# Optimization experiments

Measured on AMD Instinct MI355X. Metric: run time of the kernel, lower is better.

## Reference

```python
import jax, jax.numpy as jnp
import numpy as np
from fractions import Fraction
from math import factorial

# ---------- e3nn-convention real Wigner 3j (computed once in numpy) ----------

def _su2_cg(j1, m1, j2, m2, j3, m3):
    if m3 != m1 + m2:
        return 0.0
    vmin = int(max(-j1 + j2 + m3, -j1 + m1, 0))
    vmax = int(min(j2 + j3 + m1, j3 - j1 + j2, j3 + m3))
    f = lambda n: factorial(round(n))
    C = ((2.0 * j3 + 1.0) * Fraction(
        f(j3 + j1 - j2) * f(j3 - j1 + j2) * f(j1 + j2 - j3) * f(j3 + m3) * f(j3 - m3),
        f(j1 + j2 + j3 + 1) * f(j1 - m1) * f(j1 + m1) * f(j2 - m2) * f(j2 + m2))) ** 0.5
    S = 0
    for v in range(vmin, vmax + 1):
        S += (-1) ** int(v + j2 + m2) * Fraction(
            f(j2 + j3 + m1 - v) * f(j1 - m1 + v),
            f(v) * f(j3 - j1 + j2 - v) * f(j3 + m3 - v) * f(v + j1 - j2 - m3))
    return float(C * S)

def _q_real2complex(l):
    q = np.zeros((2 * l + 1, 2 * l + 1), dtype=complex)
    for m in range(-l, 0):
        q[l + m, l + abs(m)] = 1 / 2 ** 0.5
        q[l + m, l - abs(m)] = -1j / 2 ** 0.5
    q[l, l] = 1.0
    for m in range(1, l + 1):
        q[l + m, l + abs(m)] = (-1) ** m / 2 ** 0.5
        q[l + m, l - abs(m)] = 1j * (-1) ** m / 2 ** 0.5
    return (-1j) ** l * q

def _w3j(l1, l2, l3):
    C = np.zeros((2 * l1 + 1, 2 * l2 + 1, 2 * l3 + 1), dtype=complex)
    for m1 in range(-l1, l1 + 1):
        for m2 in range(-l2, l2 + 1):
            for m3 in range(-l3, l3 + 1):
                C[l1 + m1, l2 + m2, l3 + m3] = _su2_cg(l1, m1, l2, m2, l3, m3)
    C = np.einsum('ij,kl,mn,ikn->jlm', _q_real2complex(l1), _q_real2complex(l2),
                  np.conj(_q_real2complex(l3).T), C)
    assert np.abs(C.imag).max() < 1e-7
    C = C.real
    return C / np.linalg.norm(C)

# uuw instructions from get_feasible_tp(hidden, hidden, 0e+1e+2e): (l1, l2, l_out)
INS = [(0, 0, 0), (0, 2, 2), (1, 1, 0), (1, 1, 1), (1, 1, 2), (2, 0, 2), (2, 2, 0), (2, 2, 1), (2, 2, 2)]
W3J = {ls: jnp.asarray(_w3j(*ls), dtype=jnp.float32) for ls in set(INS)}
# change of basis of ReducedTensorProducts('ij', i='1o'): sph(0e+1e+2e) -> cart 3x3
Q_COB = jnp.asarray(np.concatenate([(2 * l + 1) ** 0.5 * _w3j(1, 1, l).transpose(2, 0, 1)
                                    for l in (0, 1, 2)], axis=0), dtype=jnp.float32)  # (9,3,3)
IN_IRR = ((128, 0), (64, 1), (32, 2))  # edge_irreps, dim 480
HID = 16                               # hidden multiplicity per l
CART = jnp.array([2, 0, 1])            # e3nn (y,z,x) -> (x,y,z)

def _split(x):
    parts, o = [], 0
    for mul, l in IN_IRR:
        d = mul * (2 * l + 1)
        parts.append(x[:, o:o + d].reshape(-1, mul, 2 * l + 1))
        o += d
    return parts

def _lin(parts, Ws):  # e3nn o3.Linear: per-l channel mix, 1/sqrt(fan_in)
    return [jnp.einsum('nui,uv->nvi', p, W) * (1.0 / np.sqrt(p.shape[1])) for p, W in zip(parts, Ws)]

def _forward(batch, x_scalar, x_spherical, WU0, WU1, WU2, WV0, WV1, WV2,
             Wg1, bg1, Wg2, bg2, Wp0, Wp1, Wp2, num_graphs):
    xs = _split(x_spherical)
    hU = _lin(xs, (WU0, WU1, WU2))  # [(N,16,1),(N,16,3),(N,16,5)]
    hV = _lin(xs, (WV0, WV1, WV2))
    w = jax.nn.silu(x_scalar @ Wg1 + bg1) @ Wg2 + bg2  # (N, 144) per-path tp weights
    outs = {0: [], 1: [], 2: []}
    for k, (l1, l2, l3) in enumerate(INS):
        wk = w[:, k * HID:(k + 1) * HID]
        coeff = float(np.sqrt((2 * l3 + 1) / HID))  # component/element norm
        outs[l3].append(coeff * jnp.einsum('nu,ijm,nui,nuj->nm', wk, W3J[(l1, l2, l3)], hU[l1], hV[l2]))
    Wp = {0: Wp0, 1: Wp1, 2: Wp2}
    sph = [jnp.einsum('num,u->nm', jnp.stack(outs[l], 1), Wp[l][:, 0]) * (1.0 / np.sqrt(len(outs[l])))
           for l in (0, 1, 2)]  # lin_out_post -> 1x0e+1x1e+1x2e
    atom_out = jnp.concatenate(sph, axis=-1)  # (N, 9)
    res_sph = jax.ops.segment_sum(atom_out, batch, num_segments=num_graphs)  # (G, 9)
    res_cart = jnp.einsum('gk,kij->gij', res_sph, Q_COB)  # (G, 3, 3)
    return res_cart[:, CART][:, :, CART]

def setup_inputs():
    key = jax.random.key(0)
    k = jax.random.split(key, 16)
    N, G = 150000, 2000
    f32 = jnp.float32
    rn = lambda kk, shp, s=1.0: jax.random.normal(kk, shp, f32) * s
    return {
        'batch': jnp.sort(jax.random.randint(k[0], (N,), 0, G)),
        'x_scalar': rn(k[1], (N, 128)),
        'x_spherical': rn(k[2], (N, 480)),
        'WU0': rn(k[3], (128, 16)), 'WU1': rn(k[4], (64, 16)), 'WU2': rn(k[5], (32, 16)),
        'WV0': rn(k[6], (128, 16)), 'WV1': rn(k[7], (64, 16)), 'WV2': rn(k[8], (32, 16)),
        'Wg1': rn(k[9], (128, 64), 128 ** -0.5), 'bg1': jnp.zeros((64,), f32),
        'Wg2': rn(k[10], (64, 144), 64 ** -0.5), 'bg2': jnp.zeros((144,), f32),
        'Wp0': rn(k[11], (3, 1)), 'Wp1': rn(k[12], (2, 1)), 'Wp2': rn(k[13], (4, 1)),
        'num_graphs': G,
    }

def reference(batch, x_scalar, x_spherical, WU0, WU1, WU2, WV0, WV1, WV2,
              Wg1, bg1, Wg2, bg2, Wp0, Wp1, Wp2, num_graphs):
    return _forward(batch, x_scalar, x_spherical, WU0, WU1, WU2, WV0, WV1, WV2,
                    Wg1, bg1, Wg2, bg2, Wp0, Wp1, Wp2, num_graphs)
```

## Files before the change

kernel.cpp:

```cpp
#include <hip/hip_runtime.h>
#include <hip/hip_bf16.h>
#include <math.h>

typedef unsigned short u16;
typedef unsigned int   u32;
typedef __attribute__((ext_vector_type(8))) short short8v;
typedef __attribute__((ext_vector_type(4))) float f32x4;

#define TILE 16

#define WS_FLAG  368
#define WS_MOK   369
#define WS_WG1   384
#define WS_WG2   8576
#define WS_WU0   17792
#define WS_WU1   19840
#define WS_WU2   20864
#define WS_WV0   21376
#define WS_WV1   23424
#define WS_WV2   24448
#define WS_BG1   24960
#define WS_BG2   25024
#define WS_C9    25168
#define WS_RES   25216

#define WSH_BG1T 88064
#define WSH_BG2T 96256
#define WSH_B0T  105472
#define WSH_B1T  109568
#define WSH_B2T  128000
#define WS_NEED_BYTES 307200

__device__ __forceinline__ float b2f(u16 u){
  return __uint_as_float(((u32)u) << 16);
}
__device__ __forceinline__ u16 f2b(float f){
  u32 x = __float_as_uint(f);
  return (u16)((x + 0x7fffu + ((x >> 16) & 1u)) >> 16);
}
__device__ __forceinline__ float ldconv(const void* p, int i, int isbf){
  return isbf ? b2f(((const u16*)p)[i]) : ((const float*)p)[i];
}

__global__ void detect_kernel(const u32* __restrict__ words, int* __restrict__ flag){
  int t = threadIdx.x;
  int cnt = 0;
  for (int i = 0; i < 16; i++){
    u32 w = words[t*16 + i];
    u32 e = (w >> 7) & 0xFF;
    cnt += (e >= 117 && e <= 137) ? 1 : 0;
  }
  #pragma unroll
  for (int m = 1; m < 64; m <<= 1) cnt += __shfl_xor(cnt, m, 64);
  if (t == 0) *flag = (cnt > 512) ? 1 : 0;
}

__device__ double factd(int n){ double r=1.0; for(int i=2;i<=n;++i) r*=(double)i; return r; }

__device__ double su2_cg(int j1,int m1,int j2,int m2,int j3,int m3){
  if (m1+m2 != m3) return 0.0;
  int vmin = max(max(-j1+j2+m3, -j1+m1), 0);
  int vmax = min(min(j2+j3+m1, j3-j1+j2), j3+m3);
  double C = sqrt((2.0*j3+1.0)
      * factd(j3+j1-j2)*factd(j3-j1+j2)*factd(j1+j2-j3)*factd(j3+m3)*factd(j3-m3)
      / (factd(j1+j2+j3+1)*factd(j1-m1)*factd(j1+m1)*factd(j2-m2)*factd(j2+m2)));
  double S = 0.0;
  for (int v=vmin; v<=vmax; ++v){
    double t = factd(j2+j3+m1-v)*factd(j1-m1+v)
             / (factd(v)*factd(j3-j1+j2-v)*factd(j3+m3-v)*factd(v+j1-j2-m3));
    S += ((v+j2+m2)&1) ? -t : t;
  }
  return C*S;
}

__device__ void qmat_lds(int l, double* qre, double* qim){
  int d = 2*l+1;
  for (int i=0;i<d*d;i++){ qre[i]=0.0; qim[i]=0.0; }
  double s = 1.0/sqrt(2.0);
  for (int m=-l; m<0; ++m){
    qre[(l+m)*d + (l-m)] = s;
    qim[(l+m)*d + (l+m)] = -s;
  }
  qre[l*d + l] = 1.0;
  for (int m=1; m<=l; ++m){
    double sgn = (m&1) ? -1.0 : 1.0;
    qre[(l+m)*d + (l+m)] = sgn*s;
    qim[(l+m)*d + (l-m)] = sgn*s;
  }
  double fr, fi;
  switch (l & 3){ case 0: fr=1; fi=0; break; case 1: fr=0; fi=-1; break;
                  case 2: fr=-1; fi=0; break; default: fr=0; fi=1; }
  for (int i=0;i<d*d;i++){
    double a=qre[i], b=qim[i];
    qre[i]=a*fr-b*fi; qim[i]=a*fi+b*fr;
  }
}

__global__ void setup_kernel(float* __restrict__ ws){
  __shared__ double q1r[25], q1i[25], q2r[25], q2i[25], q3r[25], q3i[25];
  __shared__ double red[128];
  const int L1[9]={0,0,1,1,1,2,2,2,2};
  const int L2[9]={0,2,1,1,1,0,2,2,2};
  const int L3[9]={0,2,0,1,2,2,0,1,2};
  const int OFF[9]={0,1,26,35,62,107,132,157,232};
  const int b = blockIdx.x;
  const int l1=L1[b], l2=L2[b], l3=L3[b];
  const int d1=2*l1+1, d2=2*l2+1, d3=2*l3+1;
  const int tot = d1*d2*d3;
  const int t = threadIdx.x;

  if (t==0) qmat_lds(l1, q1r, q1i);
  if (t==1) qmat_lds(l2, q2r, q2i);
  if (t==2) qmat_lds(l3, q3r, q3i);
  __syncthreads();

  double ar = 0.0;
  if (t < tot){
    const int j = t/(d2*d3), rem = t - j*(d2*d3), l = rem/d3, m = rem - l*d3;
    for (int i=0;i<d1;i++){
      double a1r=q1r[i*d1+j], a1i=q1i[i*d1+j];
      for (int k=0;k<d2;k++){
        double a2r=q2r[k*d2+l], a2i=q2i[k*d2+l];
        double t12r = a1r*a2r - a1i*a2i;
        double t12i = a1r*a2i + a1i*a2r;
        for (int n=0;n<d3;n++){
          double c = su2_cg(l1, i-l1, l2, k-l2, l3, n-l3);
          if (c==0.0) continue;
          double a3r = q3r[n*d3+m], a3i = -q3i[n*d3+m];
          ar += c*(t12r*a3r - t12i*a3i);
        }
      }
    }
  }
  red[t] = ar*ar;
  __syncthreads();
  for (int s=64; s>0; s>>=1){
    if (t < s) red[t] += red[t+s];
    __syncthreads();
  }
  double nrm = sqrt(red[0]);
  if (t < tot) ws[OFF[b] + t] = (float)(ar/nrm);
}

__global__ void convert_weights(
    const void* Wg1, const void* Wg2,
    const void* WU0, const void* WU1, const void* WU2,
    const void* WV0, const void* WV1, const void* WV2,
    const void* bg1, const void* bg2,
    const void* Wp0, const void* Wp1, const void* Wp2,
    float* __restrict__ ws)
{
  const int isbf = ((const int*)ws)[WS_FLAG];
  const int b = blockIdx.x, t = threadIdx.x;
  u16* wh = (u16*)ws;
  if (b < 10){
    const void* src[10] = {Wg1,Wg2,WU0,WU1,WU2,WV0,WV1,WV2,bg1,bg2};
    const int   sz[10]  = {8192,9216,2048,1024,512,2048,1024,512,64,144};
    const int   off[10] = {WS_WG1,WS_WG2,WS_WU0,WS_WU1,WS_WU2,WS_WV0,WS_WV1,WS_WV2,WS_BG1,WS_BG2};
    const void* s = src[b]; float* d = ws + off[b]; int n = sz[b];
    for (int i = t; i < n; i += 256) d[i] = ldconv(s, i, isbf);
  } else if (b == 10){
    if (t == 0){
      float* C9 = ws + WS_C9;
      const int l3k[9]  = {0,2,0,1,2,2,0,1,2};
      const int idxk[9] = {0,0,1,0,1,2,2,1,3};
      for (int k=0;k<9;k++){
        int l3 = l3k[k];
        const void* wp = (l3==0) ? Wp0 : (l3==1) ? Wp1 : Wp2;
        float wpv = ldconv(wp, idxk[k], isbf);
        float len = (l3==0) ? 3.f : (l3==1) ? 2.f : 4.f;
        C9[k] = sqrtf((2.f*l3 + 1.f)/16.f) * wpv * rsqrtf(len);
      }
    }
  } else if (b == 11){
    for (int i=t;i<8192;i+=256){
      int n = i >> 7, k = i & 127;
      wh[WSH_BG1T + i] = f2b(ldconv(Wg1, k*64 + n, isbf));
    }
  } else if (b == 12){
    for (int i=t;i<9216;i+=256){
      int n = i >> 6, k = i & 63;
      wh[WSH_BG2T + i] = f2b(ldconv(Wg2, k*144 + n, isbf));
    }
  } else if (b == 13){
    for (int i=t;i<4096;i+=256){
      int n = i >> 7, k = i & 127;
      float v = (n < 16) ? ldconv(WU0, k*16 + n, isbf)
                         : ldconv(WV0, k*16 + (n-16), isbf);
      wh[WSH_B0T + i] = f2b(v);
    }
  } else if (b == 14){
    for (int i=t;i<18432;i+=256){
      int n = i / 192, k = i - n*192;
      int uv = n / 48, rem = n - uv*48, ii = rem >> 4, vv = rem & 15;
      float val = 0.f;
      if (k % 3 == ii){
        int u = k / 3;
        val = ldconv(uv ? WV1 : WU1, u*16 + vv, isbf);
      }
      wh[WSH_B1T + i] = f2b(val);
    }
  } else if (b == 15){
    for (int i=t;i<25600;i+=256){
      int n = i / 160, k = i - n*160;
      int uv = n / 80, rem = n - uv*80, ii = rem >> 4, vv = rem & 15;
      float val = 0.f;
      if (k % 5 == ii){
        int u = k / 5;
        val = ldconv(uv ? WV2 : WU2, u*16 + vv, isbf);
      }
      wh[WSH_B2T + i] = f2b(val);
    }
  }
}

__global__ void probe_kernel(float* __restrict__ ws){
  __shared__ u16 A[512];
  __shared__ u16 B[512];
  int t = threadIdx.x;
  for (int i=t;i<512;i+=64){
    int m = i >> 5, k = i & 31;
    A[i] = f2b((float)(((3*m + k) % 7) - 3));
    int kk = i >> 4, n = i & 15;
    B[i] = f2b((float)(((2*kk + 5*n) % 9) - 4));
  }
  __syncthreads();
  int v = t & 15, g4 = t >> 4;
  short8v a, b;
  #pragma unroll
  for (int j=0;j<8;j++){
    a[j] = (short)A[v*32 + 8*g4 + j];
    b[j] = (short)B[(8*g4 + j)*16 + v];
  }
  f32x4 c = {0.f,0.f,0.f,0.f};
  c = __builtin_amdgcn_mfma_f32_16x16x32_bf16(a, b, c, 0, 0, 0);
  int ok = 1;
  #pragma unroll
  for (int r=0;r<4;r++){
    int row = 4*g4 + r;
    float ref = 0.f;
    for (int k=0;k<32;k++) ref += b2f(A[row*32+k]) * b2f(B[k*16+v]);
    if (fabsf(c[r] - ref) > 0.25f) ok = 0;
  }
  #pragma unroll
  for (int m=1;m<64;m<<=1) ok &= __shfl_xor(ok, m, 64);
  if (t == 0) ((int*)ws)[WS_MOK] = ok;
}

__global__ __launch_bounds__(256,3) void mfma_kernel(
    const int* __restrict__ batch,
    const void* __restrict__ xscv,
    const void* __restrict__ xspv,
    const float* __restrict__ ws,
    float* __restrict__ res,
    int N)
{
  const int isbf = ((const int*)ws)[WS_FLAG];
  const int mok  = ((const int*)ws)[WS_MOK];
  if (!(isbf && mok)) return;

  __shared__ __align__(16) u16 H1hi[4][16][72];
  __shared__ __align__(16) u16 H1lo[4][16][72];

  const int tid = threadIdx.x;
  const int wave = tid >> 6, lane = tid & 63;
  const int v = lane & 15, g4 = lane >> 4;
  const int tile = blockIdx.x*4 + wave;
  const int n0 = tile * TILE;
  if (n0 >= N) return;

  const u16* xsc = (const u16*)xscv;
  const u16* xsp = (const u16*)xspv;
  const u16* wb  = (const u16*)ws;

  int rowA = n0 + v; if (rowA >= N) rowA = N - 1;

  f32x4 accg[4];
  #pragma unroll
  for (int nt=0;nt<4;nt++) accg[nt] = (f32x4){0.f,0.f,0.f,0.f};
  {
    const u16* aP = xsc + (size_t)rowA*128 + 8*g4;
    const u16* bP = wb + WSH_BG1T + v*128 + 8*g4;
    #pragma unroll
    for (int kt=0;kt<4;kt++){
      short8v a = *(const short8v*)(aP + kt*32);
      #pragma unroll
      for (int nt=0;nt<4;nt++){
        short8v b = *(const short8v*)(bP + nt*2048 + kt*32);
        accg[nt] = __builtin_amdgcn_mfma_f32_16x16x32_bf16(a, b, accg[nt], 0, 0, 0);
      }
    }
  }
  #pragma unroll
  for (int nt=0;nt<4;nt++){
    float bb = ws[WS_BG1 + nt*16 + v];
    #pragma unroll
    for (int r=0;r<4;r++){
      float hs = accg[nt][r] + bb;
      float h  = hs / (1.f + __expf(-hs));
      u16 hi = f2b(h);
      float lo = h - b2f(hi);
      int atom = 4*g4 + r;
      H1hi[wave][atom][nt*16 + v] = hi;
      H1lo[wave][atom][nt*16 + v] = f2b(lo);
    }
  }

  f32x4 accw[9];
  #pragma unroll
  for (int nt=0;nt<9;nt++) accw[nt] = (f32x4){0.f,0.f,0.f,0.f};
  {
    const u16* hH = &H1hi[wave][v][8*g4];
    const u16* hL = &H1lo[wave][v][8*g4];
    const u16* bP = wb + WSH_BG2T + v*64 + 8*g4;
    #pragma unroll
    for (int kt=0;kt<2;kt++){
      short8v ah = *(const short8v*)(hH + kt*32);
      short8v al = *(const short8v*)(hL + kt*32);
      #pragma unroll
      for (int nt=0;nt<9;nt++){
        short8v b = *(const short8v*)(bP + nt*1024 + kt*32);
        accw[nt] = __builtin_amdgcn_mfma_f32_16x16x32_bf16(ah, b, accw[nt], 0, 0, 0);
        accw[nt] = __builtin_amdgcn_mfma_f32_16x16x32_bf16(al, b, accw[nt], 0, 0, 0);
      }
    }
  }
  float wkv[9][4];
  #pragma unroll
  for (int nt=0;nt<9;nt++){
    float bb = ws[WS_BG2 + nt*16 + v];
    float c9 = ws[WS_C9 + nt];
    #pragma unroll
    for (int r=0;r<4;r++) wkv[nt][r] = (accw[nt][r] + bb) * c9;
  }

  const u16* spA = xsp + (size_t)rowA*480 + 8*g4;

  f32x4 acc0[2];
  #pragma unroll
  for (int nt=0;nt<2;nt++) acc0[nt] = (f32x4){0.f,0.f,0.f,0.f};
  {
    const u16* bP = wb + WSH_B0T + v*128 + 8*g4;
    #pragma unroll
    for (int kt=0;kt<4;kt++){
      short8v a = *(const short8v*)(spA + kt*32);
      #pragma unroll
      for (int nt=0;nt<2;nt++){
        short8v b = *(const short8v*)(bP + nt*2048 + kt*32);
        acc0[nt] = __builtin_amdgcn_mfma_f32_16x16x32_bf16(a, b, acc0[nt], 0, 0, 0);
      }
    }
  }
  f32x4 accA[6];
  #pragma unroll
  for (int nt=0;nt<6;nt++) accA[nt] = (f32x4){0.f,0.f,0.f,0.f};
  {
    const u16* bP = wb + WSH_B1T + v*192 + 8*g4;
    #pragma unroll
    for (int kt=0;kt<6;kt++){
      short8v a = *(const short8v*)(spA + 128 + kt*32);
      #pragma unroll
      for (int nt=0;nt<6;nt++){
        short8v b = *(const short8v*)(bP + nt*3072 + kt*32);
        accA[nt] = __builtin_amdgcn_mfma_f32_16x16x32_bf16(a, b, accA[nt], 0, 0, 0);
      }
    }
  }
  f32x4 accB[10];
  #pragma unroll
  for (int nt=0;nt<10;nt++) accB[nt] = (f32x4){0.f,0.f,0.f,0.f};
  {
    const u16* bP = wb + WSH_B2T + v*160 + 8*g4;
    #pragma unroll
    for (int kt=0;kt<5;kt++){
      short8v a = *(const short8v*)(spA + 320 + kt*32);
      #pragma unroll
      for (int nt=0;nt<10;nt++){
        short8v b = *(const short8v*)(bP + nt*2560 + kt*32);
        accB[nt] = __builtin_amdgcn_mfma_f32_16x16x32_bf16(a, b, accB[nt], 0, 0, 0);
      }
    }
  }

  int bidr[4];
  #pragma unroll
  for (int r=0;r<4;r++){
    int n = n0 + 4*g4 + r;
    bidr[r] = (n < N) ? batch[n] : -1;
  }

  const float r128 = 0.088388347648318447f;
  const float r64  = 0.125f;
  const float r32  = 0.17677669529663689f;
  const float* J = ws;
  float pend[9];
  int pg = -1;

  #pragma unroll
  for (int r=0;r<4;r++){
    float hu0 = acc0[0][r]*r128, hv0 = acc0[1][r]*r128;
    float hu1[3], hv1[3], hu2[5], hv2[5];
    #pragma unroll
    for (int i=0;i<3;i++){ hu1[i] = accA[i][r]*r64; hv1[i] = accA[3+i][r]*r64; }
    #pragma unroll
    for (int i=0;i<5;i++){ hu2[i] = accB[i][r]*r32; hv2[i] = accB[5+i][r]*r32; }

    float t9[9] = {0,0,0,0,0,0,0,0,0};
    t9[0] += wkv[0][r]*J[0]*hu0*hv0;
    {
      float cw = wkv[1][r]*hu0;
      #pragma unroll
      for (int m=0;m<5;m++){
        float s=0.f;
        #pragma unroll
        for (int j=0;j<5;j++) s += J[1 + j*5 + m]*hv2[j];
        t9[4+m] += cw*s;
      }
    }
    {
      float s=0.f;
      #pragma unroll
      for (int i=0;i<3;i++)
        #pragma unroll
        for (int j=0;j<3;j++) s += J[26 + i*3 + j]*hu1[i]*hv1[j];
      t9[0] += wkv[2][r]*s;
    }
    {
      float sm[3]={0,0,0};
      #pragma unroll
      for (int i=0;i<3;i++)
        #pragma unroll
        for (int j=0;j<3;j++){
          float p = hu1[i]*hv1[j];
          #pragma unroll
          for (int m=0;m<3;m++) sm[m] += J[35 + (i*3+j)*3 + m]*p;
        }
      #pragma unroll
      for (int m=0;m<3;m++) t9[1+m] += wkv[3][r]*sm[m];
    }
    {
      float sm[5]={0,0,0,0,0};
      #pragma unroll
      for (int i=0;i<3;i++)
        #pragma unroll
        for (int j=0;j<3;j++){
          float p = hu1[i]*hv1[j];
          #pragma unroll
          for (int m=0;m<5;m++) sm[m] += J[62 + (i*3+j)*5 + m]*p;
        }
      #pragma unroll
      for (int m=0;m<5;m++) t9[4+m] += wkv[4][r]*sm[m];
    }
    {
      float cw = wkv[5][r]*hv0;
      #pragma unroll
      for (int m=0;m<5;m++){
        float s=0.f;
        #pragma unroll
        for (int i=0;i<5;i++) s += J[107 + i*5 + m]*hu2[i];
        t9[4+m] += cw*s;
      }
    }
    {
      float s=0.f;
      #pragma unroll
      for (int i=0;i<5;i++)
        #pragma unroll
        for (int j=0;j<5;j++) s += J[132 + i*5 + j]*hu2[i]*hv2[j];
      t9[0] += wkv[6][r]*s;
    }
    {
      float sm[3]={0,0,0};
      #pragma unroll
      for (int i=0;i<5;i++)
        #pragma unroll
        for (int j=0;j<5;j++){
          float p = hu2[i]*hv2[j];
          #pragma unroll
          for (int m=0;m<3;m++) sm[m] += J[157 + (i*5+j)*3 + m]*p;
        }
      #pragma unroll
      for (int m=0;m<3;m++) t9[1+m] += wkv[7][r]*sm[m];
    }
    {
      float sm[5]={0,0,0,0,0};
      #pragma unroll
      for (int i=0;i<5;i++)
        #pragma unroll
        for (int j=0;j<5;j++){
          float p = hu2[i]*hv2[j];
          #pragma unroll
          for (int m=0;m<5;m++) sm[m] += J[232 + (i*5+j)*5 + m]*p;
        }
      #pragma unroll
      for (int m=0;m<5;m++) t9[4+m] += wkv[8][r]*sm[m];
    }

    #pragma unroll
    for (int mask=1; mask<16; mask<<=1){
      #pragma unroll
      for (int s=0;s<9;s++) t9[s] += __shfl_xor(t9[s], mask, 64);
    }
    if (v == 0){
      int n = n0 + 4*g4 + r;
      if (n < N){
        int g = bidr[r];
        if (g == pg){
          #pragma unroll
          for (int s=0;s<9;s++) pend[s] += t9[s];
        } else {
          if (pg >= 0){
            float* rp = res + (size_t)pg*9;
            #pragma unroll
            for (int s=0;s<9;s++) atomicAdd(&rp[s], pend[s]);
          }
          pg = g;
          #pragma unroll
          for (int s=0;s<9;s++) pend[s] = t9[s];
        }
      }
    }
  }
  if (v == 0 && pg >= 0){
    float* rp = res + (size_t)pg*9;
    #pragma unroll
    for (int s=0;s<9;s++) atomicAdd(&rp[s], pend[s]);
  }
}

__device__ __forceinline__ void load8_bf16(const u16* p, float* dst){
  uint4 vv = *reinterpret_cast<const uint4*>(p);
  u32 w[4] = {vv.x, vv.y, vv.z, vv.w};
  #pragma unroll
  for (int q=0;q<4;q++){
    dst[2*q]   = __uint_as_float((w[q] & 0xffffu) << 16);
    dst[2*q+1] = __uint_as_float(w[q] & 0xffff0000u);
  }
}
__device__ __forceinline__ void load8_f32(const float* p, float* dst){
  float4 v0 = *reinterpret_cast<const float4*>(p);
  float4 v1 = *reinterpret_cast<const float4*>(p+4);
  dst[0]=v0.x; dst[1]=v0.y; dst[2]=v0.z; dst[3]=v0.w;
  dst[4]=v1.x; dst[5]=v1.y; dst[6]=v1.z; dst[7]=v1.w;
}

__global__ __launch_bounds__(256) void main_kernel(
    const int* __restrict__ batch,
    const void* __restrict__ xscv,
    const void* __restrict__ xspv,
    const float* __restrict__ ws,
    float* __restrict__ res,
    int N)
{
  {
    const int fb = ((const int*)ws)[WS_FLAG];
    const int mk = ((const int*)ws)[WS_MOK];
    if (fb && mk) return;
  }
  __shared__ float s_xsph[TILE][481];
  __shared__ float s_w[TILE][144];
  __shared__ float s_uni[4624];
  __shared__ float s_w3j[357];
  __shared__ float s_bg1[64];
  __shared__ float s_bg2[144];
  __shared__ float s_C[9];
  __shared__ int   s_batch[TILE];

  float (*s_xs)[128] = reinterpret_cast<float(*)[128]>(s_uni);
  float (*s_h1)[64]  = reinterpret_cast<float(*)[64]>(s_uni + 2048);
  float (*s_hU)[144] = reinterpret_cast<float(*)[144]>(s_uni);
  float (*s_hV)[144] = reinterpret_cast<float(*)[144]>(s_uni + 2304);

  const int tid  = threadIdx.x;
  const int wave = tid >> 6;
  const int lane = tid & 63;
  const int n0   = blockIdx.x * TILE;
  const int isbf = ((const int*)ws)[WS_FLAG];

  const float* wsWg1 = ws + WS_WG1;
  const float* wsWg2 = ws + WS_WG2;
  const float* wsWU0 = ws + WS_WU0;
  const float* wsWU1 = ws + WS_WU1;
  const float* wsWU2 = ws + WS_WU2;
  const float* wsWV0 = ws + WS_WV0;
  const float* wsWV1 = ws + WS_WV1;
  const float* wsWV2 = ws + WS_WV2;

  if (tid < TILE){ int n = n0 + tid; s_batch[tid] = (n < N) ? batch[n] : -1; }
  if (tid < 64)  s_bg1[tid] = ws[WS_BG1 + tid];
  if (tid < 144) s_bg2[tid] = ws[WS_BG2 + tid];
  if (tid < 9)   s_C[tid]   = ws[WS_C9 + tid];
  for (int i = tid; i < 357; i += 256) s_w3j[i] = ws[i];
  {
    int base = tid*8, row = base >> 7, col = base & 127;
    int n = n0 + row;
    if (n < N){
      if (isbf) load8_bf16((const u16*)xscv + (size_t)n*128 + col, &s_xs[row][col]);
      else      load8_f32 ((const float*)xscv + (size_t)n*128 + col, &s_xs[row][col]);
    } else { for (int q=0;q<8;q++) s_xs[row][col+q] = 0.f; }
  }
  {
    for (int it = tid; it < 960; it += 256){
      int base = it*8, row = base/480, col = base - row*480;
      int n = n0 + row;
      if (n < N){
        if (isbf) load8_bf16((const u16*)xspv + (size_t)n*480 + col, &s_xsph[row][col]);
        else      load8_f32 ((const float*)xspv + (size_t)n*480 + col, &s_xsph[row][col]);
      } else { for (int q=0;q<8;q++) s_xsph[row][col+q] = 0.f; }
    }
  }
  __syncthreads();

  {
    const int a0 = wave*4;
    float acc0=s_bg1[lane], acc1=acc0, acc2=acc0, acc3=acc0;
    for (int c=0;c<128;c++){
      float wv = wsWg1[c*64 + lane];
      acc0 += s_xs[a0+0][c]*wv;
      acc1 += s_xs[a0+1][c]*wv;
      acc2 += s_xs[a0+2][c]*wv;
      acc3 += s_xs[a0+3][c]*wv;
    }
    s_h1[a0+0][lane] = acc0/(1.f+__expf(-acc0));
    s_h1[a0+1][lane] = acc1/(1.f+__expf(-acc1));
    s_h1[a0+2][lane] = acc2/(1.f+__expf(-acc2));
    s_h1[a0+3][lane] = acc3/(1.f+__expf(-acc3));
  }
  __syncthreads();

  {
    const int a0 = wave*4;
    float acc[4][3];
    #pragma unroll
    for (int t=0;t<4;t++){
      acc[t][0] = s_bg2[lane];
      acc[t][1] = s_bg2[64+lane];
      acc[t][2] = (lane<16) ? s_bg2[128+lane] : 0.f;
    }
    for (int c=0;c<64;c++){
      float w0 = wsWg2[c*144 + lane];
      float w1 = wsWg2[c*144 + 64 + lane];
      float w2 = (lane<16) ? wsWg2[c*144 + 128 + lane] : 0.f;
      #pragma unroll
      for (int t=0;t<4;t++){
        float h = s_h1[a0+t][c];
        acc[t][0] += h*w0; acc[t][1] += h*w1; acc[t][2] += h*w2;
      }
    }
    #pragma unroll
    for (int t=0;t<4;t++){
      s_w[a0+t][lane]    = acc[t][0];
      s_w[a0+t][64+lane] = acc[t][1];
      if (lane < 16) s_w[a0+t][128+lane] = acc[t][2];
    }
  }
  __syncthreads();

  {
    const int a = tid >> 4, v = tid & 15;
    const float r128 = 0.088388347648318447f;
    const float r64  = 0.125f;
    const float r32  = 0.17677669529663689f;
    {
      float aU=0.f, aV=0.f;
      for (int u=0;u<128;u++){
        float x = s_xsph[a][u];
        aU += x*wsWU0[u*16+v];
        aV += x*wsWV0[u*16+v];
      }
      s_hU[a][v] = aU*r128; s_hV[a][v] = aV*r128;
    }
    {
      float aU[3]={0,0,0}, aV[3]={0,0,0};
      for (int u=0;u<64;u++){
        float wu = wsWU1[u*16+v], wv = wsWV1[u*16+v];
        #pragma unroll
        for (int i=0;i<3;i++){
          float x = s_xsph[a][128 + u*3 + i];
          aU[i] += x*wu; aV[i] += x*wv;
        }
      }
      #pragma unroll
      for (int i=0;i<3;i++){ s_hU[a][16+v*3+i]=aU[i]*r64; s_hV[a][16+v*3+i]=aV[i]*r64; }
    }
    {
      float aU[5]={0,0,0,0,0}, aV[5]={0,0,0,0,0};
      for (int u=0;u<32;u++){
        float wu = wsWU2[u*16+v], wv = wsWV2[u*16+v];
        #pragma unroll
        for (int i=0;i<5;i++){
          float x = s_xsph[a][320 + u*5 + i];
          aU[i] += x*wu; aV[i] += x*wv;
        }
      }
      #pragma unroll
      for (int i=0;i<5;i++){ s_hU[a][64+v*5+i]=aU[i]*r32; s_hV[a][64+v*5+i]=aV[i]*r32; }
    }
  }
  __syncthreads();

  {
    const int a = tid >> 4, u = tid & 15;
    float hu0 = s_hU[a][u], hv0 = s_hV[a][u];
    float hu1[3], hv1[3], hu2[5], hv2[5];
    #pragma unroll
    for (int i=0;i<3;i++){ hu1[i]=s_hU[a][16+u*3+i]; hv1[i]=s_hV[a][16+u*3+i]; }
    #pragma unroll
    for (int i=0;i<5;i++){ hu2[i]=s_hU[a][64+u*5+i]; hv2[i]=s_hV[a][64+u*5+i]; }
    float wk[9];
    #pragma unroll
    for (int k=0;k<9;k++) wk[k] = s_w[a][k*16+u];

    const float* J = s_w3j;
    float t9[9] = {0,0,0,0,0,0,0,0,0};

    t9[0] += s_C[0]*wk[0]*J[0]*hu0*hv0;
    {
      float cw = s_C[1]*wk[1]*hu0;
      #pragma unroll
      for (int m=0;m<5;m++){
        float s=0.f;
        #pragma unroll
        for (int j=0;j<5;j++) s += J[1 + j*5 + m]*hv2[j];
        t9[4+m] += cw*s;
      }
    }
    {
      float s=0.f;
      #pragma unroll
      for (int i=0;i<3;i++)
        #pragma unroll
        for (int j=0;j<3;j++) s += J[26 + i*3 + j]*hu1[i]*hv1[j];
      t9[0] += s_C[2]*wk[2]*s;
    }
    {
      float sm[3]={0,0,0};
      #pragma unroll
      for (int i=0;i<3;i++)
        #pragma unroll
        for (int j=0;j<3;j++){
          float p = hu1[i]*hv1[j];
          #pragma unroll
          for (int m=0;m<3;m++) sm[m] += J[35 + (i*3+j)*3 + m]*p;
        }
      float c = s_C[3]*wk[3];
      #pragma unroll
      for (int m=0;m<3;m++) t9[1+m] += c*sm[m];
    }
    {
      float sm[5]={0,0,0,0,0};
      #pragma unroll
      for (int i=0;i<3;i++)
        #pragma unroll
        for (int j=0;j<3;j++){
          float p = hu1[i]*hv1[j];
          #pragma unroll
          for (int m=0;m<5;m++) sm[m] += J[62 + (i*3+j)*5 + m]*p;
        }
      float c = s_C[4]*wk[4];
      #pragma unroll
      for (int m=0;m<5;m++) t9[4+m] += c*sm[m];
    }
    {
      float cw = s_C[5]*wk[5]*hv0;
      #pragma unroll
      for (int m=0;m<5;m++){
        float s=0.f;
        #pragma unroll
        for (int i=0;i<5;i++) s += J[107 + i*5 + m]*hu2[i];
        t9[4+m] += cw*s;
      }
    }
    {
      float s=0.f;
      #pragma unroll
      for (int i=0;i<5;i++)
        #pragma unroll
        for (int j=0;j<5;j++) s += J[132 + i*5 + j]*hu2[i]*hv2[j];
      t9[0] += s_C[6]*wk[6]*s;
    }
    {
      float sm[3]={0,0,0};
      #pragma unroll
      for (int i=0;i<5;i++)
        #pragma unroll
        for (int j=0;j<5;j++){
          float p = hu2[i]*hv2[j];
          #pragma unroll
          for (int m=0;m<3;m++) sm[m] += J[157 + (i*5+j)*3 + m]*p;
        }
      float c = s_C[7]*wk[7];
      #pragma unroll
      for (int m=0;m<3;m++) t9[1+m] += c*sm[m];
    }
    {
      float sm[5]={0,0,0,0,0};
      #pragma unroll
      for (int i=0;i<5;i++)
        #pragma unroll
        for (int j=0;j<5;j++){
          float p = hu2[i]*hv2[j];
          #pragma unroll
          for (int m=0;m<5;m++) sm[m] += J[232 + (i*5+j)*5 + m]*p;
        }
      float c = s_C[8]*wk[8];
      #pragma unroll
      for (int m=0;m<5;m++) t9[4+m] += c*sm[m];
    }

    #pragma unroll
    for (int mask=1; mask<16; mask<<=1){
      #pragma unroll
      for (int s=0;s<9;s++) t9[s] += __shfl_xor(t9[s], mask, 64);
    }
    if (u == 0 && (n0 + a) < N){
      int g = s_batch[a];
      float* r = res + (size_t)g*9;
      #pragma unroll
      for (int s=0;s<9;s++) atomicAdd(&r[s], t9[s]);
    }
  }
}

__global__ void finish_kernel(const float* __restrict__ res,
                              const float* __restrict__ ws,
                              void* __restrict__ out, int G)
{
  int idx = blockIdx.x*256 + threadIdx.x;
  if (idx >= G*9) return;
  const int isbf = ((const int*)ws)[WS_FLAG];
  int g = idx/9, s = idx - g*9;
  int a = s/3, b = s - a*3;
  const int cart[3] = {2,0,1};
  int ca = cart[a], cb = cart[b];
  const float s3 = 1.7320508075688772f, s5 = 2.2360679774997896f;
  const float* r = res + (size_t)g*9;
  float acc = r[0]*ws[26 + ca*3 + cb];
  #pragma unroll
  for (int m=0;m<3;m++) acc += r[1+m]*s3*ws[35 + (ca*3+cb)*3 + m];
  #pragma unroll
  for (int m=0;m<5;m++) acc += r[4+m]*s5*ws[62 + (ca*3+cb)*5 + m];
  if (isbf) ((__hip_bfloat16*)out)[idx] = __float2bfloat16(acc);
  else      ((float*)out)[idx] = acc;
}

extern "C" void kernel_launch(void* const* d_in, const int* in_sizes, int n_in,
                              void* d_out, int out_size, void* d_ws, size_t ws_size,
                              hipStream_t stream) {
  const int* batch = (const int*)d_in[0];
  const void* xsc = d_in[1];
  const void* xsp = d_in[2];

  const int N = in_sizes[0];
  const int G = out_size / 9;

  float* ws  = (float*)d_ws;
  float* res = ws + WS_RES;

  const bool big = (ws_size >= (size_t)WS_NEED_BYTES) && (G <= 2090);

  hipMemsetAsync(res, 0, (size_t)G*9*sizeof(float), stream);
  hipMemsetAsync(ws + WS_MOK, 0, sizeof(int), stream);
  detect_kernel<<<1, 64, 0, stream>>>((const u32*)xsp, (int*)(ws + WS_FLAG));
  setup_kernel<<<9, 128, 0, stream>>>(ws);
  convert_weights<<<big ? 16 : 11, 256, 0, stream>>>(d_in[9], d_in[11],
                                          d_in[3], d_in[4], d_in[5],
                                          d_in[6], d_in[7], d_in[8],
                                          d_in[10], d_in[12],
                                          d_in[13], d_in[14], d_in[15],
                                          ws);
  if (big){
    probe_kernel<<<1, 64, 0, stream>>>(ws);
    mfma_kernel<<<(N + 63)/64, 256, 0, stream>>>(batch, xsc, xsp, ws, res, N);
  }

  int nb = (N + TILE - 1) / TILE;
  main_kernel<<<nb, 256, 0, stream>>>(batch, xsc, xsp, ws, res, N);

  finish_kernel<<<(G*9 + 255)/256, 256, 0, stream>>>(res, ws, d_out, G);
}
```

Baseline: 1.162 ms.

## Replace block-diagonal l1/l2 weight matrices with strided-gather MFMA on compact tables

The l=1 and l=2 projections used zero-padded block-diagonal B matrices (6x6 and 10x5 MFMA tiles), most of whose entries were zeros. They now gather each m-component of the spherical input with a strided load and multiply by a compact shared U/V weight table, cutting MFMA count and B-table traffic. The bf16 tables are built by a new kernel that copies raw bf16 values without conversion, and they live at a smaller workspace offset, so the workspace-size gate is dropped and the MFMA path always launches. Launch bounds go from 3 to 2 blocks per SM. The A loads become scalar strided gathers, which may cost memory efficiency.

After: 1.160 ms. About the same (-0.2%).

```diff
diff --git a/kernel.cpp b/kernel.cpp
--- a/kernel.cpp
+++ b/kernel.cpp
@@ -24,12 +24,11 @@
 #define WS_C9    25168
 #define WS_RES   25216
 
-#define WSH_BG1T 88064
-#define WSH_BG2T 96256
-#define WSH_B0T  105472
-#define WSH_B1T  109568
-#define WSH_B2T  128000
-#define WS_NEED_BYTES 307200
+#define WT_BG1T 768
+#define WT_BG2T 8960
+#define WT_B0T  18176
+#define WT_B1T  22272
+#define WT_B2T  24320
 
 __device__ __forceinline__ float b2f(u16 u){
   return __uint_as_float(((u32)u) << 16);
@@ -152,64 +151,22 @@
 {
   const int isbf = ((const int*)ws)[WS_FLAG];
   const int b = blockIdx.x, t = threadIdx.x;
-  u16* wh = (u16*)ws;
   if (b < 10){
     const void* src[10] = {Wg1,Wg2,WU0,WU1,WU2,WV0,WV1,WV2,bg1,bg2};
     const int   sz[10]  = {8192,9216,2048,1024,512,2048,1024,512,64,144};
     const int   off[10] = {WS_WG1,WS_WG2,WS_WU0,WS_WU1,WS_WU2,WS_WV0,WS_WV1,WS_WV2,WS_BG1,WS_BG2};
     const void* s = src[b]; float* d = ws + off[b]; int n = sz[b];
     for (int i = t; i < n; i += 256) d[i] = ldconv(s, i, isbf);
-  } else if (b == 10){
-    if (t == 0){
-      float* C9 = ws + WS_C9;
-      const int l3k[9]  = {0,2,0,1,2,2,0,1,2};
-      const int idxk[9] = {0,0,1,0,1,2,2,1,3};
-      for (int k=0;k<9;k++){
-        int l3 = l3k[k];
-        const void* wp = (l3==0) ? Wp0 : (l3==1) ? Wp1 : Wp2;
-        float wpv = ldconv(wp, idxk[k], isbf);
-        float len = (l3==0) ? 3.f : (l3==1) ? 2.f : 4.f;
-        C9[k] = sqrtf((2.f*l3 + 1.f)/16.f) * wpv * rsqrtf(len);
-      }
-    }
-  } else if (b == 11){
-    for (int i=t;i<8192;i+=256){
-      int n = i >> 7, k = i & 127;
-      wh[WSH_BG1T + i] = f2b(ldconv(Wg1, k*64 + n, isbf));
-    }
-  } else if (b == 12){
-    for (int i=t;i<9216;i+=256){
-      int n = i >> 6, k = i & 63;
-      wh[WSH_BG2T + i] = f2b(ldconv(Wg2, k*144 + n, isbf));
-    }
-  } else if (b == 13){
-    for (int i=t;i<4096;i+=256){
-      int n = i >> 7, k = i & 127;
-      float v = (n < 16) ? ldconv(WU0, k*16 + n, isbf)
-                         : ldconv(WV0, k*16 + (n-16), isbf);
-      wh[WSH_B0T + i] = f2b(v);
-    }
-  } else if (b == 14){
-    for (int i=t;i<18432;i+=256){
-      int n = i / 192, k = i - n*192;
-      int uv = n / 48, rem = n - uv*48, ii = rem >> 4, vv = rem & 15;
-      float val = 0.f;
-      if (k % 3 == ii){
-        int u = k / 3;
-        val = ldconv(uv ? WV1 : WU1, u*16 + vv, isbf);
-      }
-      wh[WSH_B1T + i] = f2b(val);
-    }
-  } else if (b == 15){
-    for (int i=t;i<25600;i+=256){
-      int n = i / 160, k = i - n*160;
-      int uv = n / 80, rem = n - uv*80, ii = rem >> 4, vv = rem & 15;
-      float val = 0.f;
-      if (k % 5 == ii){
-        int u = k / 5;
-        val = ldconv(uv ? WV2 : WU2, u*16 + vv, isbf);
-      }
-      wh[WSH_B2T + i] = f2b(val);
+  } else if (b == 10 && t == 0){
+    float* C9 = ws + WS_C9;
+    const int l3k[9]  = {0,2,0,1,2,2,0,1,2};
+    const int idxk[9] = {0,0,1,0,1,2,2,1,3};
+    for (int k=0;k<9;k++){
+      int l3 = l3k[k];
+      const void* wp = (l3==0) ? Wp0 : (l3==1) ? Wp1 : Wp2;
+      float wpv = ldconv(wp, idxk[k], isbf);
+      float len = (l3==0) ? 3.f : (l3==1) ? 2.f : 4.f;
+      C9[k] = sqrtf((2.f*l3 + 1.f)/16.f) * wpv * rsqrtf(len);
     }
   }
 }
@@ -247,7 +204,49 @@
   if (t == 0) ((int*)ws)[WS_MOK] = ok;
 }
 
-__global__ __launch_bounds__(256,3) void mfma_kernel(
+__global__ void convert_tables(
+    const void* Wg1, const void* Wg2,
+    const void* WU0, const void* WU1, const void* WU2,
+    const void* WV0, const void* WV1, const void* WV2,
+    float* __restrict__ ws)
+{
+  const int isbf = ((const int*)ws)[WS_FLAG];
+  const int mok  = ((const int*)ws)[WS_MOK];
+  if (!(isbf && mok)) return;
+  u16* wh = (u16*)ws;
+  const int b = blockIdx.x, t = threadIdx.x;
+  if (b == 0){
+    for (int i=t;i<8192;i+=256){
+      int n = i >> 7, k = i & 127;
+      wh[WT_BG1T + i] = ((const u16*)Wg1)[k*64 + n];
+    }
+  } else if (b == 1){
+    for (int i=t;i<9216;i+=256){
+      int n = i >> 6, k = i & 63;
+      wh[WT_BG2T + i] = ((const u16*)Wg2)[k*144 + n];
+    }
+  } else if (b == 2){
+    for (int i=t;i<4096;i+=256){
+      int n = i >> 7, k = i & 127;
+      wh[WT_B0T + i] = (n < 16) ? ((const u16*)WU0)[k*16 + n]
+                                : ((const u16*)WV0)[k*16 + (n-16)];
+    }
+  } else if (b == 3){
+    for (int i=t;i<2048;i+=256){
+      int n = i >> 6, u = i & 63;
+      wh[WT_B1T + i] = (n < 16) ? ((const u16*)WU1)[u*16 + n]
+                                : ((const u16*)WV1)[u*16 + (n-16)];
+    }
+  } else if (b == 4){
+    for (int i=t;i<1024;i+=256){
+      int n = i >> 5, u = i & 31;
+      wh[WT_B2T + i] = (n < 16) ? ((const u16*)WU2)[u*16 + n]
+                                : ((const u16*)WV2)[u*16 + (n-16)];
+    }
+  }
+}
+
+__global__ __launch_bounds__(256,2) void mfma_kernel(
     const int* __restrict__ batch,
     const void* __restrict__ xscv,
     const void* __restrict__ xspv,
@@ -280,7 +279,7 @@
   for (int nt=0;nt<4;nt++) accg[nt] = (f32x4){0.f,0.f,0.f,0.f};
   {
     const u16* aP = xsc + (size_t)rowA*128 + 8*g4;
-    const u16* bP = wb + WSH_BG1T + v*128 + 8*g4;
+    const u16* bP = wb + WT_BG1T + v*128 + 8*g4;
     #pragma unroll
     for (int kt=0;kt<4;kt++){
       short8v a = *(const short8v*)(aP + kt*32);
@@ -312,7 +311,7 @@
   {
     const u16* hH = &H1hi[wave][v][8*g4];
     const u16* hL = &H1lo[wave][v][8*g4];
-    const u16* bP = wb + WSH_BG2T + v*64 + 8*g4;
+    const u16* bP = wb + WT_BG2T + v*64 + 8*g4;
     #pragma unroll
     for (int kt=0;kt<2;kt++){
       short8v ah = *(const short8v*)(hH + kt*32);
@@ -334,16 +333,17 @@
     for (int r=0;r<4;r++) wkv[nt][r] = (accw[nt][r] + bb) * c9;
   }
 
-  const u16* spA = xsp + (size_t)rowA*480 + 8*g4;
+  const u16* spRow = xsp + (size_t)rowA*480;
 
   f32x4 acc0[2];
   #pragma unroll
   for (int nt=0;nt<2;nt++) acc0[nt] = (f32x4){0.f,0.f,0.f,0.f};
   {
-    const u16* bP = wb + WSH_B0T + v*128 + 8*g4;
+    const u16* aP = spRow + 8*g4;
+    const u16* bP = wb + WT_B0T + v*128 + 8*g4;
     #pragma unroll
     for (int kt=0;kt<4;kt++){
-      short8v a = *(const short8v*)(spA + kt*32);
+      short8v a = *(const short8v*)(aP + kt*32);
       #pragma unroll
       for (int nt=0;nt<2;nt++){
         short8v b = *(const short8v*)(bP + nt*2048 + kt*32);
@@ -351,34 +351,47 @@
       }
     }
   }
+
   f32x4 accA[6];
   #pragma unroll
   for (int nt=0;nt<6;nt++) accA[nt] = (f32x4){0.f,0.f,0.f,0.f};
   {
-    const u16* bP = wb + WSH_B1T + v*192 + 8*g4;
-    #pragma unroll
-    for (int kt=0;kt<6;kt++){
-      short8v a = *(const short8v*)(spA + 128 + kt*32);
-      #pragma unroll
-      for (int nt=0;nt<6;nt++){
-        short8v b = *(const short8v*)(bP + nt*3072 + kt*32);
-        accA[nt] = __builtin_amdgcn_mfma_f32_16x16x32_bf16(a, b, accA[nt], 0, 0, 0);
-      }
-    }
-  }
+    const u16* bU = wb + WT_B1T + v*64 + 8*g4;
+    const u16* bV = wb + WT_B1T + (16+v)*64 + 8*g4;
+    short8v bu0 = *(const short8v*)(bU);
+    short8v bu1 = *(const short8v*)(bU + 32);
+    short8v bv0 = *(const short8v*)(bV);
+    short8v bv1 = *(const short8v*)(bV + 32);
+    #pragma unroll
+    for (int i=0;i<3;i++){
+      #pragma unroll
+      for (int kt=0;kt<2;kt++){
+        const u16* ap = spRow + 128 + i + 3*(32*kt + 8*g4);
+        short8v a;
+        #pragma unroll
+        for (int j=0;j<8;j++) a[j] = (short)ap[3*j];
+        short8v bu = kt ? bu1 : bu0;
+        short8v bv = kt ? bv1 : bv0;
+        accA[i]   = __builtin_amdgcn_mfma_f32_16x16x32_bf16(a, bu, accA[i],   0, 0, 0);
+        accA[3+i] = __builtin_amdgcn_mfma_f32_16x16x32_bf16(a, bv, accA[3+i], 0, 0, 0);
+      }
+    }
+  }
+
   f32x4 accB[10];
   #pragma unroll
   for (int nt=0;nt<10;nt++) accB[nt] = (f32x4){0.f,0.f,0.f,0.f};
   {
-    const u16* bP = wb + WSH_B2T + v*160 + 8*g4;
-    #pragma unroll
-    for (int kt=0;kt<5;kt++){
-      short8v a = *(const short8v*)(spA + 320 + kt*32);
-      #pragma unroll
-      for (int nt=0;nt<10;nt++){
-        short8v b = *(const short8v*)(bP + nt*2560 + kt*32);
-        accB[nt] = __builtin_amdgcn_mfma_f32_16x16x32_bf16(a, b, accB[nt], 0, 0, 0);
-      }
+    short8v b2u = *(const short8v*)(wb + WT_B2T + v*32 + 8*g4);
+    short8v b2v = *(const short8v*)(wb + WT_B2T + (16+v)*32 + 8*g4);
+    #pragma unroll
+    for (int i=0;i<5;i++){
+      const u16* ap = spRow + 320 + i + 5*(8*g4);
+      short8v a;
+      #pragma unroll
+      for (int j=0;j<8;j++) a[j] = (short)ap[5*j];
+      accB[i]   = __builtin_amdgcn_mfma_f32_16x16x32_bf16(a, b2u, accB[i],   0, 0, 0);
+      accB[5+i] = __builtin_amdgcn_mfma_f32_16x16x32_bf16(a, b2v, accB[5+i], 0, 0, 0);
     }
   }
 
@@ -857,22 +870,22 @@
   float* ws  = (float*)d_ws;
   float* res = ws + WS_RES;
 
-  const bool big = (ws_size >= (size_t)WS_NEED_BYTES) && (G <= 2090);
-
   hipMemsetAsync(res, 0, (size_t)G*9*sizeof(float), stream);
   hipMemsetAsync(ws + WS_MOK, 0, sizeof(int), stream);
   detect_kernel<<<1, 64, 0, stream>>>((const u32*)xsp, (int*)(ws + WS_FLAG));
   setup_kernel<<<9, 128, 0, stream>>>(ws);
-  convert_weights<<<big ? 16 : 11, 256, 0, stream>>>(d_in[9], d_in[11],
+  convert_weights<<<11, 256, 0, stream>>>(d_in[9], d_in[11],
                                           d_in[3], d_in[4], d_in[5],
                                           d_in[6], d_in[7], d_in[8],
                                           d_in[10], d_in[12],
                                           d_in[13], d_in[14], d_in[15],
                                           ws);
-  if (big){
-    probe_kernel<<<1, 64, 0, stream>>>(ws);
-    mfma_kernel<<<(N + 63)/64, 256, 0, stream>>>(batch, xsc, xsp, ws, res, N);
-  }
+  probe_kernel<<<1, 64, 0, stream>>>(ws);
+  convert_tables<<<5, 256, 0, stream>>>(d_in[9], d_in[11],
+                                        d_in[3], d_in[4], d_in[5],
+                                        d_in[6], d_in[7], d_in[8],
+                                        ws);
+  mfma_kernel<<<(N + 63)/64, 256, 0, stream>>>(batch, xsc, xsp, ws, res, N);
 
   int nb = (N + TILE - 1) / TILE;
   main_kernel<<<nb, 256, 0, stream>>>(batch, xsc, xsp, ws, res, N);
```
